# Performance work log

Measured on AMD Instinct MI355X. Metric: run time of the kernel, lower is better.

The kernel has to match this reference:

```python
import jax, jax.numpy as jnp
import numpy as np


def _phase_idx(phase):
    t = 4.0 * phase
    i1 = jnp.mod(jnp.floor(t).astype(jnp.int32), 4)
    i0 = jnp.mod(i1 - 1, 4)
    i2 = jnp.mod(i1 + 1, 4)
    i3 = jnp.mod(i1 + 2, 4)
    w = jnp.mod(t, 1.0)  # fmod(t,1) for t>=0
    return w, i0, i1, i2, i3


def _cubic(a0, a1, a2, a3, w):
    # Catmull-Rom spline blend; a* have shape (B, ...), w broadcastable
    return (a1
            + w * (0.5 * a2 - 0.5 * a0)
            + w * w * (a0 - 2.5 * a1 + 2.0 * a2 - 0.5 * a3)
            + w * w * w * (1.5 * a1 - 1.5 * a2 + 0.5 * a3 - 0.5 * a0))


def setup_inputs() -> dict:
    key = jax.random.key(0)
    ks = jax.random.split(key, 8)
    B = 4096
    dims = [128, 256, 256, 128]

    def kaiming(k, shape):
        fan_in = shape[1]
        bound = np.sqrt(6.0 / fan_in)
        return jax.random.uniform(k, shape, jnp.float32, -bound, bound)

    inp = {
        "x": jax.random.normal(ks[0], (B, dims[0]), jnp.float32),
        "phase": jax.random.uniform(ks[1], (B,), jnp.float32),
    }
    for i in range(3):
        inp[f"w{i}"] = kaiming(ks[2 + i], (4, dims[i], dims[i + 1]))
        inp[f"b{i}"] = jnp.zeros((4, 1, dims[i + 1]), jnp.float32)
    return inp


def reference(x, phase, w0, b0, w1, b1, w2, b2):
    ws = [w0, w1, w2]
    bs = [b0, b1, b2]
    w, i0, i1, i2, i3 = _phase_idx(phase)
    w3 = w[:, None, None]  # (B,1,1) for weights and biases
    n = len(ws)
    for li in range(n):
        pw, pb = ws[li], bs[li]
        # per-sample interpolated weight (B, in, out) and bias (B, 1, out)
        weight = _cubic(pw[i0], pw[i1], pw[i2], pw[i3], w3)
        bias = _cubic(pb[i0], pb[i1], pb[i2], pb[i3], w3)
        x = jnp.einsum("bi,bio->bo", x, weight) + bias[:, 0, :]
        if li < n - 1:  # activation_at_last=False
            x = jax.nn.elu(x)
    return x
```

## Files before the change

kernel.cpp:

```cpp
#include <hip/hip_runtime.h>
#include <hip/hip_bf16.h>
#include <math.h>


typedef __attribute__((ext_vector_type(8))) short bf16x8;
typedef __attribute__((ext_vector_type(4))) float f32x4;

#define LDS_A0 0
#define LDS_A1 4096
#define LDS_A2 12288
#define LDS_CB 20480
#define LDS_B  21504
#define LDS_TOT (21504 + 131072)

#define VMW4()  asm volatile("s_waitcnt vmcnt(4)" ::: "memory")
#define VMW0()  asm volatile("s_waitcnt vmcnt(0)" ::: "memory")
#define LGKM0() asm volatile("s_waitcnt lgkmcnt(0)" ::: "memory")

static __device__ __forceinline__ void bar_keep_vmcnt() {
  asm volatile("s_waitcnt lgkmcnt(0)" ::: "memory");
  __builtin_amdgcn_s_barrier();
  asm volatile("" ::: "memory");
}

typedef const __attribute__((address_space(1))) unsigned char* gp1_t;
typedef __attribute__((address_space(3))) unsigned char* lp3_t;
static __device__ __forceinline__ void gl_lds16(const void* g, void* l) {
  __builtin_amdgcn_global_load_lds((gp1_t)g, (lp3_t)l, 16, 0, 0);
}

#define STAGE(sb, ci, slot) do {                                       \
    const unsigned short* _s = (sb) + (ci) * 2048;                     \
    char* _d = myB + (slot) * 4096;                                    \
    gl_lds16(_s,        _d);                                           \
    gl_lds16(_s +  512, _d + 1024);                                    \
    gl_lds16(_s + 1024, _d + 2048);                                    \
    gl_lds16(_s + 1536, _d + 3072);                                    \
  } while (0)

static __device__ __forceinline__ unsigned short f2bf(float f) {
  union { float f; unsigned int u; } v; v.f = f;
  unsigned int r = v.u + 0x7fffu + ((v.u >> 16) & 1u);
  return (unsigned short)(r >> 16);
}

static __device__ __forceinline__ void catmull(float ph, float c[4]) {
  float t = 4.0f * ph;
  float ft = floorf(t);
  int i1 = ((int)ft) & 3;
  float w = t - ft;
  float w2 = w * w, w3 = w2 * w;
  float r0 = -0.5f * w + w2 - 0.5f * w3;
  float r1 = 1.0f - 2.5f * w2 + 1.5f * w3;
  float r2 = 0.5f * w + 2.0f * w2 - 1.5f * w3;
  float r3 = -0.5f * w2 + 0.5f * w3;
  c[(i1 + 3) & 3] = r0;
  c[i1]           = r1;
  c[(i1 + 1) & 3] = r2;
  c[(i1 + 2) & 3] = r3;
}

#define TPAD 66
__global__ __launch_bounds__(256) void k_pack(
    const float* __restrict__ w0, const float* __restrict__ w1,
    const float* __restrict__ w2, unsigned short* __restrict__ t0,
    unsigned short* __restrict__ t1, unsigned short* __restrict__ t2) {
  __shared__ float tile[4 * 32 * TPAD];
  const int u = blockIdx.x;
  const int t = threadIdx.x;

  const float* W; unsigned short* T;
  int q, ci8, KO, Ostr, nsub, cgmul, cgstride, cisub;
  if (u < 16) {
    q = u >> 2; ci8 = u & 3;
    W = w0; T = t0; KO = 128 * 256; Ostr = 256; nsub = 4;
    cgmul = 8192; cgstride = 1; cisub = ci8;
  } else if (u < 48) {
    const int uu = u - 16; q = uu >> 3; ci8 = uu & 7;
    W = w1; T = t1; KO = 256 * 256; Ostr = 256; nsub = 4;
    cgmul = 16384; cgstride = 1; cisub = ci8;
  } else {
    const int uu = u - 48; q = uu >> 3; ci8 = uu & 7;
    W = w2; T = t2; KO = 256 * 128; Ostr = 128; nsub = 4;
    cgmul = 16384; cgstride = 2; cisub = ci8;
  }
  const int kbase = ci8 * 32;
  const int obase = q * 64;

#pragma unroll
  for (int p = 0; p < 8; ++p) {
    const int f4 = p * 256 + t;
    const int a = f4 >> 9;
    const int k = (f4 >> 4) & 31;
    const int o4 = f4 & 15;
    const float4 v = *(const float4*)(W + (size_t)a * KO +
                                      (size_t)(kbase + k) * Ostr + obase + o4 * 4);
    float* d = tile + a * (32 * TPAD) + k * TPAD + o4 * 4;
    d[0] = v.x; d[1] = v.y; d[2] = v.z; d[3] = v.w;
  }
  __syncthreads();

  const int a = t >> 6, w = t & 63, col = w & 15, quad = w >> 4;
#pragma unroll
  for (int s = 0; s < nsub; ++s) {
    const float* src = tile + a * (32 * TPAD) + (quad * 8) * TPAD + s * 16 + col;
    bf16x8 v;
#pragma unroll
    for (int j = 0; j < 8; ++j) v[j] = (short)f2bf(src[j * TPAD]);
    size_t dst;
    if (u < 48) {
      dst = (size_t)(q * 4 + s) * (size_t)cgmul + (size_t)cisub * 2048 + a * 512 + w * 8;
    } else {
      const int cg = q * 4 + s, kh = ci8 >> 2, ci4 = ci8 & 3;
      dst = (size_t)(cg * 2 + kh) * 8192 + (size_t)ci4 * 2048 + a * 512 + w * 8;
    }
    *(bf16x8*)(T + dst) = v;
  }
}

static __device__ __forceinline__ void epi_mid(f32x4 a0, f32x4 a1, f32x4 a2, f32x4 a3,
                                               const float bv[4], const float* cbf,
                                               int colg, int quad, char* outBuf) {
  const int g = colg >> 3;
  const int j2 = (colg & 7) * 2;
#pragma unroll
  for (int r = 0; r < 4; ++r) {
    const int m = quad * 4 + r;
    const float4 c = *(const float4*)(cbf + m * 4);
    float y = c.x * (a0[r] + bv[0]) + c.y * (a1[r] + bv[1]) +
              c.z * (a2[r] + bv[2]) + c.w * (a3[r] + bv[3]);
    float a = y > 0.0f ? y : (__expf(y) - 1.0f);
    *(unsigned short*)(outBuf + m * 512 + (((g ^ (m & 15)) << 4) + j2)) = f2bf(a);
  }
}

#define MFMA4()                                                            \
  acc0 = __builtin_amdgcn_mfma_f32_16x16x32_bf16(av, bv0, acc0, 0, 0, 0);  \
  acc1 = __builtin_amdgcn_mfma_f32_16x16x32_bf16(av, bv1, acc1, 0, 0, 0);  \
  acc2 = __builtin_amdgcn_mfma_f32_16x16x32_bf16(av, bv2, acc2, 0, 0, 0);  \
  acc3 = __builtin_amdgcn_mfma_f32_16x16x32_bf16(av, bv3, acc3, 0, 0, 0)

#define LOADB()                                                \
  bf16x8 bv0 = *(const bf16x8*)(bs + bOff);                    \
  bf16x8 bv1 = *(const bf16x8*)(bs + 1024 + bOff);             \
  bf16x8 bv2 = *(const bf16x8*)(bs + 2048 + bOff);             \
  bf16x8 bv3 = *(const bf16x8*)(bs + 3072 + bOff)

__global__ __launch_bounds__(1024, 4) void k_fused(
    const float* __restrict__ x, const float* __restrict__ phase,
    const unsigned short* __restrict__ Wt0, const float* __restrict__ b0,
    const unsigned short* __restrict__ Wt1, const float* __restrict__ b1,
    const unsigned short* __restrict__ Wt2, const float* __restrict__ b2,
    float* __restrict__ out) {
  __shared__ __align__(1024) char smem[LDS_TOT];

  const int tid = threadIdx.x;
  const int lane = tid & 63;
  const int wid = tid >> 6;
  const int col = lane & 15;
  const int quad = lane >> 4;
  const int m0 = blockIdx.x * 16;
  const int colg = wid * 16 + col;
  const int cg = wid & 7, kh = wid >> 3;
  const int colg2 = cg * 16 + col;
  const int hi16 = (col & 12) << 4;
  const int lb = (quad ^ (col & 3)) << 4;
  const int bOff = lane * 16;

  char* myB = smem + LDS_B + wid * 8192;
  float* cbf = (float*)(smem + LDS_CB);

  const unsigned short* sb0 = Wt0 + (size_t)wid * 8192 + lane * 8;
  const unsigned short* sb1 = Wt1 + (size_t)wid * 16384 + lane * 8;
  const unsigned short* sb2 = Wt2 + (size_t)(cg * 2 + kh) * 8192 + lane * 8;

  float4 xv = {0.f, 0.f, 0.f, 0.f};
  if (tid < 512)
    xv = *(const float4*)(x + (size_t)(m0 + (tid >> 5)) * 128 + (tid & 31) * 4);

  float bva[4], bvb[4], bvc[4];
#pragma unroll
  for (int k = 0; k < 4; ++k) {
    bva[k] = b0[k * 256 + colg];
    bvb[k] = b1[k * 256 + colg];
    bvc[k] = b2[k * 128 + colg2];
  }

  if (tid < 16) {
    float c[4];
    catmull(phase[m0 + tid], c);
    cbf[tid * 4 + 0] = c[0]; cbf[tid * 4 + 1] = c[1];
    cbf[tid * 4 + 2] = c[2]; cbf[tid * 4 + 3] = c[3];
  }

  STAGE(sb0, 0, 0);
  STAGE(sb0, 1, 1);

  if (tid < 512) {
    const int row = tid >> 5, seg = tid & 31;
    const int g = seg >> 1, h = seg & 1;
    short4 hv;
    hv.x = (short)f2bf(xv.x); hv.y = (short)f2bf(xv.y);
    hv.z = (short)f2bf(xv.z); hv.w = (short)f2bf(xv.w);
    *(short4*)(smem + LDS_A0 + row * 256 + ((g ^ (row & 15)) << 4) + h * 8) = hv;
  }
  bar_keep_vmcnt();

  f32x4 acc0, acc1, acc2, acc3;

  {
    acc0 = acc1 = acc2 = acc3 = (f32x4){0.f, 0.f, 0.f, 0.f};
    const char* aL = smem + LDS_A0 + col * 256 + lb;
#pragma unroll
    for (int i = 0; i < 4; ++i) {
      VMW4();
      const char* bs = myB + (i & 1) * 4096;
      bf16x8 av = *(const bf16x8*)(aL + ((i << 6) ^ hi16));
      LOADB();
      LGKM0();
      if (i == 0)      STAGE(sb0, 2, 0);
      else if (i == 1) STAGE(sb0, 3, 1);
      else if (i == 2) STAGE(sb1, 0, 0);
      else             STAGE(sb1, 1, 1);
      MFMA4();
    }
    epi_mid(acc0, acc1, acc2, acc3, bva, cbf, colg, quad, smem + LDS_A1);
  }
  bar_keep_vmcnt();

  {
    acc0 = acc1 = acc2 = acc3 = (f32x4){0.f, 0.f, 0.f, 0.f};
    const char* aL = smem + LDS_A1 + col * 512 + lb;
#pragma unroll
    for (int i = 0; i < 8; ++i) {
      VMW4();
      const char* bs = myB + (i & 1) * 4096;
      bf16x8 av = *(const bf16x8*)(aL + ((i << 6) ^ hi16));
      LOADB();
      LGKM0();
      if (i < 6)       STAGE(sb1, i + 2, i & 1);
      else if (i == 6) STAGE(sb2, 0, 0);
      else             STAGE(sb2, 1, 1);
      MFMA4();
    }
    epi_mid(acc0, acc1, acc2, acc3, bvb, cbf, colg, quad, smem + LDS_A2);
  }
  bar_keep_vmcnt();

  {
    acc0 = acc1 = acc2 = acc3 = (f32x4){0.f, 0.f, 0.f, 0.f};
    const char* aL = smem + LDS_A2 + col * 512 + kh * 256 + lb;
#pragma unroll
    for (int i = 0; i < 4; ++i) {
      if (i < 3) { VMW4(); } else { VMW0(); }
      const char* bs = myB + (i & 1) * 4096;
      bf16x8 av = *(const bf16x8*)(aL + ((i << 6) ^ hi16));
      LOADB();
      if (i < 2) {
        LGKM0();
        if (i == 0) STAGE(sb2, 2, 0);
        else        STAGE(sb2, 3, 1);
      }
      MFMA4();
    }

    float part[4];
#pragma unroll
    for (int r = 0; r < 4; ++r) {
      const int m = quad * 4 + r;
      const float4 c = *(const float4*)(cbf + m * 4);
      part[r] = c.x * acc0[r] + c.y * acc1[r] + c.z * acc2[r] + c.w * acc3[r];
    }

    bar_keep_vmcnt();
    float* red = (float*)(smem + LDS_B);
    if (kh) {
#pragma unroll
      for (int r = 0; r < 4; ++r)
        red[cg * 272 + (quad * 4 + r) * 17 + col] = part[r];
    }
    bar_keep_vmcnt();
    if (!kh) {
#pragma unroll
      for (int r = 0; r < 4; ++r) {
        const int m = quad * 4 + r;
        const float4 c = *(const float4*)(cbf + m * 4);
        float y = part[r] + red[cg * 272 + m * 17 + col] +
                  c.x * bvc[0] + c.y * bvc[1] + c.z * bvc[2] + c.w * bvc[3];
        out[(size_t)(m0 + m) * 128 + colg2] = y;
      }
    }
  }
}

extern "C" void kernel_launch(void* const* d_in, const int* in_sizes, int n_in,
                              void* d_out, int out_size, void* d_ws, size_t ws_size,
                              hipStream_t stream) {
  const float* x     = (const float*)d_in[0];
  const float* phase = (const float*)d_in[1];
  const float* w0    = (const float*)d_in[2];
  const float* b0    = (const float*)d_in[3];
  const float* w1    = (const float*)d_in[4];
  const float* b1    = (const float*)d_in[5];
  const float* w2    = (const float*)d_in[6];
  const float* b2    = (const float*)d_in[7];
  float* out = (float*)d_out;

  char* ws = (char*)d_ws;
  unsigned short* Wt0 = (unsigned short*)ws;
  unsigned short* Wt1 = (unsigned short*)(ws + 262144);
  unsigned short* Wt2 = (unsigned short*)(ws + 262144 + 524288);

  k_pack<<<64, 256, 0, stream>>>(w0, w1, w2, Wt0, Wt1, Wt2);
  k_fused<<<256, 1024, 0, stream>>>(x, phase, Wt0, b0, Wt1, b1, Wt2, b2, out);
}
```

Measured before the change: 83.07 us.

## Prefetch weight chunks into registers instead of LDS via global_load_lds

Replaces the per-wave double-buffered global-to-LDS staging of packed bf16 weight chunks with a 3-deep register prefetch ring, loading B fragments straight from global memory into VGPRs. This cuts LDS use from about 150KB to about 29KB and drops the manual vmcnt/lgkmcnt waits, leaving the compiler to schedule the waits. The reduction buffer gets its own LDS region, which removes one barrier. The cost is higher register pressure (12 extra bf16x8 vectors) under a 1024-thread launch bound, plus reliance on the compiler placing the waits well.

```diff
diff --git a/kernel.cpp b/kernel.cpp
--- a/kernel.cpp
+++ b/kernel.cpp
@@ -6,37 +6,18 @@
 typedef __attribute__((ext_vector_type(8))) short bf16x8;
 typedef __attribute__((ext_vector_type(4))) float f32x4;
 
-#define LDS_A0 0
-#define LDS_A1 4096
-#define LDS_A2 12288
-#define LDS_CB 20480
-#define LDS_B  21504
-#define LDS_TOT (21504 + 131072)
-
-#define VMW4()  asm volatile("s_waitcnt vmcnt(4)" ::: "memory")
-#define VMW0()  asm volatile("s_waitcnt vmcnt(0)" ::: "memory")
-#define LGKM0() asm volatile("s_waitcnt lgkmcnt(0)" ::: "memory")
-
-static __device__ __forceinline__ void bar_keep_vmcnt() {
+#define LDS_A0  0
+#define LDS_A1  4096
+#define LDS_A2  12288
+#define LDS_CB  20480
+#define LDS_RED 20736
+#define LDS_TOT (20736 + 8704)
+
+static __device__ __forceinline__ void bar_lgkm() {
   asm volatile("s_waitcnt lgkmcnt(0)" ::: "memory");
   __builtin_amdgcn_s_barrier();
   asm volatile("" ::: "memory");
 }
-
-typedef const __attribute__((address_space(1))) unsigned char* gp1_t;
-typedef __attribute__((address_space(3))) unsigned char* lp3_t;
-static __device__ __forceinline__ void gl_lds16(const void* g, void* l) {
-  __builtin_amdgcn_global_load_lds((gp1_t)g, (lp3_t)l, 16, 0, 0);
-}
-
-#define STAGE(sb, ci, slot) do {                                       \
-    const unsigned short* _s = (sb) + (ci) * 2048;                     \
-    char* _d = myB + (slot) * 4096;                                    \
-    gl_lds16(_s,        _d);                                           \
-    gl_lds16(_s +  512, _d + 1024);                                    \
-    gl_lds16(_s + 1024, _d + 2048);                                    \
-    gl_lds16(_s + 1536, _d + 3072);                                    \
-  } while (0)
 
 static __device__ __forceinline__ unsigned short f2bf(float f) {
   union { float f; unsigned int u; } v; v.f = f;
@@ -70,19 +51,19 @@
   const int t = threadIdx.x;
 
   const float* W; unsigned short* T;
-  int q, ci8, KO, Ostr, nsub, cgmul, cgstride, cisub;
+  int q, ci8, KO, Ostr, nsub, cgmul, cisub;
   if (u < 16) {
     q = u >> 2; ci8 = u & 3;
     W = w0; T = t0; KO = 128 * 256; Ostr = 256; nsub = 4;
-    cgmul = 8192; cgstride = 1; cisub = ci8;
+    cgmul = 8192; cisub = ci8;
   } else if (u < 48) {
     const int uu = u - 16; q = uu >> 3; ci8 = uu & 7;
     W = w1; T = t1; KO = 256 * 256; Ostr = 256; nsub = 4;
-    cgmul = 16384; cgstride = 1; cisub = ci8;
+    cgmul = 16384; cisub = ci8;
   } else {
     const int uu = u - 48; q = uu >> 3; ci8 = uu & 7;
     W = w2; T = t2; KO = 256 * 128; Ostr = 128; nsub = 4;
-    cgmul = 16384; cgstride = 2; cisub = ci8;
+    cgmul = 16384; cisub = ci8;
   }
   const int kbase = ci8 * 32;
   const int obase = q * 64;
@@ -134,17 +115,24 @@
   }
 }
 
+#define LOADCH(sb, ci, sl) do {                                        \
+    pre[sl][0] = *(const bf16x8*)((sb) + (ci) * 2048);                 \
+    pre[sl][1] = *(const bf16x8*)((sb) + (ci) * 2048 + 512);           \
+    pre[sl][2] = *(const bf16x8*)((sb) + (ci) * 2048 + 1024);          \
+    pre[sl][3] = *(const bf16x8*)((sb) + (ci) * 2048 + 1536);          \
+  } while (0)
+
+#define ISSUE(c, sl) do {                                              \
+    if ((c) < 4)       LOADCH(sb0, (c), sl);                           \
+    else if ((c) < 12) LOADCH(sb1, (c) - 4, sl);                       \
+    else if ((c) < 16) LOADCH(sb2, (c) - 12, sl);                      \
+  } while (0)
+
 #define MFMA4()                                                            \
   acc0 = __builtin_amdgcn_mfma_f32_16x16x32_bf16(av, bv0, acc0, 0, 0, 0);  \
   acc1 = __builtin_amdgcn_mfma_f32_16x16x32_bf16(av, bv1, acc1, 0, 0, 0);  \
   acc2 = __builtin_amdgcn_mfma_f32_16x16x32_bf16(av, bv2, acc2, 0, 0, 0);  \
   acc3 = __builtin_amdgcn_mfma_f32_16x16x32_bf16(av, bv3, acc3, 0, 0, 0)
-
-#define LOADB()                                                \
-  bf16x8 bv0 = *(const bf16x8*)(bs + bOff);                    \
-  bf16x8 bv1 = *(const bf16x8*)(bs + 1024 + bOff);             \
-  bf16x8 bv2 = *(const bf16x8*)(bs + 2048 + bOff);             \
-  bf16x8 bv3 = *(const bf16x8*)(bs + 3072 + bOff)
 
 __global__ __launch_bounds__(1024, 4) void k_fused(
     const float* __restrict__ x, const float* __restrict__ phase,
@@ -165,9 +153,7 @@
   const int colg2 = cg * 16 + col;
   const int hi16 = (col & 12) << 4;
   const int lb = (quad ^ (col & 3)) << 4;
-  const int bOff = lane * 16;
-
-  char* myB = smem + LDS_B + wid * 8192;
+
   float* cbf = (float*)(smem + LDS_CB);
 
   const unsigned short* sb0 = Wt0 + (size_t)wid * 8192 + lane * 8;
@@ -185,6 +171,11 @@
     bvb[k] = b1[k * 256 + colg];
     bvc[k] = b2[k * 128 + colg2];
   }
+
+  bf16x8 pre[3][4];
+  LOADCH(sb0, 0, 0);
+  LOADCH(sb0, 1, 1);
+  LOADCH(sb0, 2, 2);
 
   if (tid < 16) {
     float c[4];
@@ -192,9 +183,6 @@
     cbf[tid * 4 + 0] = c[0]; cbf[tid * 4 + 1] = c[1];
     cbf[tid * 4 + 2] = c[2]; cbf[tid * 4 + 3] = c[3];
   }
-
-  STAGE(sb0, 0, 0);
-  STAGE(sb0, 1, 1);
 
   if (tid < 512) {
     const int row = tid >> 5, seg = tid & 31;
@@ -204,7 +192,7 @@
     hv.z = (short)f2bf(xv.z); hv.w = (short)f2bf(xv.w);
     *(short4*)(smem + LDS_A0 + row * 256 + ((g ^ (row & 15)) << 4) + h * 8) = hv;
   }
-  bar_keep_vmcnt();
+  bar_lgkm();
 
   f32x4 acc0, acc1, acc2, acc3;
 
@@ -213,54 +201,45 @@
     const char* aL = smem + LDS_A0 + col * 256 + lb;
 #pragma unroll
     for (int i = 0; i < 4; ++i) {
-      VMW4();
-      const char* bs = myB + (i & 1) * 4096;
+      const int sl = i % 3;
+      bf16x8 bv0 = pre[sl][0], bv1 = pre[sl][1],
+             bv2 = pre[sl][2], bv3 = pre[sl][3];
+      ISSUE(i + 3, sl);
       bf16x8 av = *(const bf16x8*)(aL + ((i << 6) ^ hi16));
-      LOADB();
-      LGKM0();
-      if (i == 0)      STAGE(sb0, 2, 0);
-      else if (i == 1) STAGE(sb0, 3, 1);
-      else if (i == 2) STAGE(sb1, 0, 0);
-      else             STAGE(sb1, 1, 1);
       MFMA4();
     }
     epi_mid(acc0, acc1, acc2, acc3, bva, cbf, colg, quad, smem + LDS_A1);
   }
-  bar_keep_vmcnt();
+  bar_lgkm();
 
   {
     acc0 = acc1 = acc2 = acc3 = (f32x4){0.f, 0.f, 0.f, 0.f};
     const char* aL = smem + LDS_A1 + col * 512 + lb;
 #pragma unroll
     for (int i = 0; i < 8; ++i) {
-      VMW4();
-      const char* bs = myB + (i & 1) * 4096;
+      const int s = i + 4;
+      const int sl = s % 3;
+      bf16x8 bv0 = pre[sl][0], bv1 = pre[sl][1],
+             bv2 = pre[sl][2], bv3 = pre[sl][3];
+      ISSUE(s + 3, sl);
       bf16x8 av = *(const bf16x8*)(aL + ((i << 6) ^ hi16));
-      LOADB();
-      LGKM0();
-      if (i < 6)       STAGE(sb1, i + 2, i & 1);
-      else if (i == 6) STAGE(sb2, 0, 0);
-      else             STAGE(sb2, 1, 1);
       MFMA4();
     }
     epi_mid(acc0, acc1, acc2, acc3, bvb, cbf, colg, quad, smem + LDS_A2);
   }
-  bar_keep_vmcnt();
+  bar_lgkm();
 
   {
     acc0 = acc1 = acc2 = acc3 = (f32x4){0.f, 0.f, 0.f, 0.f};
     const char* aL = smem + LDS_A2 + col * 512 + kh * 256 + lb;
 #pragma unroll
     for (int i = 0; i < 4; ++i) {
-      if (i < 3) { VMW4(); } else { VMW0(); }
-      const char* bs = myB + (i & 1) * 4096;
+      const int s = i + 12;
+      const int sl = s % 3;
+      bf16x8 bv0 = pre[sl][0], bv1 = pre[sl][1],
+             bv2 = pre[sl][2], bv3 = pre[sl][3];
+      ISSUE(s + 3, sl);
       bf16x8 av = *(const bf16x8*)(aL + ((i << 6) ^ hi16));
-      LOADB();
-      if (i < 2) {
-        LGKM0();
-        if (i == 0) STAGE(sb2, 2, 0);
-        else        STAGE(sb2, 3, 1);
-      }
       MFMA4();
     }
 
@@ -272,14 +251,13 @@
       part[r] = c.x * acc0[r] + c.y * acc1[r] + c.z * acc2[r] + c.w * acc3[r];
     }
 
-    bar_keep_vmcnt();
-    float* red = (float*)(smem + LDS_B);
+    float* red = (float*)(smem + LDS_RED);
     if (kh) {
 #pragma unroll
       for (int r = 0; r < 4; ++r)
         red[cg * 272 + (quad * 4 + r) * 17 + col] = part[r];
     }
-    bar_keep_vmcnt();
+    bar_lgkm();
     if (!kh) {
 #pragma unroll
       for (int r = 0; r < 4; ++r) {
```

Result: no change. 82.93 us (-0.2%).
